# Performance work log

Hardware: AMD Instinct MI355X
Metric: run time of the kernel (lower is better)

Reference implementation:

```python
import jax, jax.numpy as jnp
import numpy as np

DIM = 1024
HIDDEN = 2048
NUM_EXPERTS = 8
TOP_K = 2


def setup_inputs() -> dict:
    key = jax.random.key(0)
    ks = jax.random.split(key, 6)
    scale = 0.02
    x = jax.random.normal(ks[0], (2, 4096, DIM), dtype=jnp.float32)
    # router: Linear(dim, num_experts, bias=False) -> weight [E, d]
    router_w = jax.random.normal(ks[1], (NUM_EXPERTS, DIM), dtype=jnp.float32) * scale
    # per-expert MLP: Linear(d, h) -> w1 [E, h, d], b1 [E, h]; Linear(h, d) -> w2 [E, d, h], b2 [E, d]
    w1 = jax.random.normal(ks[2], (NUM_EXPERTS, HIDDEN, DIM), dtype=jnp.float32) * scale
    b1 = jnp.zeros((NUM_EXPERTS, HIDDEN), dtype=jnp.float32)
    w2 = jax.random.normal(ks[3], (NUM_EXPERTS, DIM, HIDDEN), dtype=jnp.float32) * scale
    b2 = jnp.zeros((NUM_EXPERTS, DIM), dtype=jnp.float32)
    return {"x": x, "router_w": router_w, "w1": w1, "b1": b1, "w2": w2, "b2": b2}


def reference(x, router_w, w1, b1, w2, b2):
    b, s, d = x.shape
    xf = x.reshape(-1, d)                              # [T, d]
    logits = xf @ router_w.T                           # [T, E]
    all_probs = jax.nn.softmax(logits, axis=-1)
    topk_logits, topk_inds = jax.lax.top_k(logits, TOP_K)   # [T, K]
    topk_probs = jax.nn.softmax(topk_logits, axis=-1)
    E = router_w.shape[0]
    onehot = jax.nn.one_hot(topk_inds, E, dtype=xf.dtype)   # [T, K, E]
    # combine weights per (token, expert); zero where expert not selected
    gate = jnp.einsum('tke,tk->te', onehot, topk_probs)     # [T, E]
    # load-balancing auxiliary loss
    f_i = onehot.mean(axis=(0, 1))                          # [E]
    P_i = all_probs.mean(axis=0)                            # [E]
    aux_loss = E * jnp.sum(f_i * P_i)
    # dense per-expert MLP, weighted combine (dropout=0 / eval mode)
    out = jnp.zeros_like(xf)
    for e in range(E):  # fixed small loop over experts
        h = jax.nn.gelu(xf @ w1[e].T + b1[e], approximate=False)  # exact GELU (torch default)
        y = h @ w2[e].T + b2[e]
        out = out + gate[:, e:e + 1] * y
    return out.reshape(b, s, d), aux_loss
```

## Files before the change

### kernel.cpp

```cpp
#include <hip/hip_runtime.h>


#define TOKS 8192
#define DIMD 1024
#define HID  2048
#define NE   8

#define OFF_COUNTS   0
#define OFF_OFFSETS  64
#define OFF_CURSORS  128
#define OFF_TILEOFF  192
#define OFF_TOPKI    256
#define OFF_TOPKG    (OFF_TOPKI + TOKS*2*4)
#define OFF_BLKPS    (OFF_TOPKG + TOKS*2*4)
#define OFF_ATOK     (OFF_BLKPS + 2048*NE*4)
#define OFF_AGATE    (OFF_ATOK + TOKS*2*4)
#define OFF_PINV     (OFF_AGATE + TOKS*2*4)
#define OFF_XG       (1u << 20)
#define XG_ROWS      (TOKS*2 + 256)
#define OFF_W1B      (OFF_XG  + (size_t)XG_ROWS * DIMD * 2)
#define OFF_W2B      (OFF_W1B + (size_t)NE * HID * DIMD * 2)
#define OFF_H        (OFF_W2B + (size_t)NE * DIMD * HID * 2)
#define OFF_Y        (OFF_H   + (size_t)XG_ROWS * HID * 2)

typedef __bf16 bf16x8 __attribute__((ext_vector_type(8)));
typedef float  floatx4 __attribute__((ext_vector_type(4)));

__device__ __forceinline__ float bf2f(unsigned short u) {
    return __uint_as_float(((unsigned)u) << 16);
}
__device__ __forceinline__ unsigned short f2bf(float f) {
    unsigned u = __float_as_uint(f);
    unsigned r = (u + 0x7FFFu + ((u >> 16) & 1u)) >> 16;
    return (unsigned short)r;
}

#define GLOBAL_AS(p) ((const __attribute__((address_space(1))) unsigned int*)(p))
#define LDS_AS(p)    ((__attribute__((address_space(3))) unsigned int*)(p))

__device__ __forceinline__ int xcd_remap(int bid, int nwg) {
    int xcd = bid & 7, pos = bid >> 3;
    int q = nwg >> 3, r = nwg & 7;
    int start = (xcd < r) ? xcd * (q + 1) : r * (q + 1) + (xcd - r) * q;
    return start + pos;
}

__global__ void convert_w_kernel(const float4* __restrict__ w1,
                                 ushort4* __restrict__ w1b, int n1,
                                 const float4* __restrict__ w2,
                                 ushort4* __restrict__ w2b, int n2) {
    int i = blockIdx.x * blockDim.x + threadIdx.x;
    int stride = gridDim.x * blockDim.x;
    int ntot = n1 + n2;
    for (; i < ntot; i += stride) {
        float4 v; ushort4 o;
        if (i < n1) v = w1[i]; else v = w2[i - n1];
        o.x = f2bf(v.x); o.y = f2bf(v.y); o.z = f2bf(v.z); o.w = f2bf(v.w);
        if (i < n1) w1b[i] = o; else w2b[i - n1] = o;
    }
}

__global__ __launch_bounds__(256) void router_kernel(
    const float* __restrict__ x, const float* __restrict__ rw,
    int* __restrict__ topki, float* __restrict__ topkg,
    float* __restrict__ blkps)
{
    int wave = threadIdx.x >> 6;
    int lane = threadIdx.x & 63;
    int t = blockIdx.x * 4 + wave;
    const float* xt = x + (size_t)t * DIMD;

    float acc[NE];
#pragma unroll
    for (int e = 0; e < NE; e++) acc[e] = 0.f;
    for (int i = 0; i < DIMD / 64; i++) {
        float xv = xt[lane + 64 * i];
#pragma unroll
        for (int e = 0; e < NE; e++) acc[e] += xv * rw[e * DIMD + lane + 64 * i];
    }
#pragma unroll
    for (int off = 32; off > 0; off >>= 1) {
#pragma unroll
        for (int e = 0; e < NE; e++) acc[e] += __shfl_down(acc[e], off);
    }

    __shared__ float ps[4][NE];
    if (lane == 0) {
        float m = acc[0];
#pragma unroll
        for (int e = 1; e < NE; e++) m = fmaxf(m, acc[e]);
        float ex[NE], s = 0.f;
#pragma unroll
        for (int e = 0; e < NE; e++) { ex[e] = expf(acc[e] - m); s += ex[e]; }
        float inv = 1.f / s;
#pragma unroll
        for (int e = 0; e < NE; e++) ps[wave][e] = ex[e] * inv;

        int i0 = 0; float l0 = acc[0];
#pragma unroll
        for (int e = 1; e < NE; e++) if (acc[e] > l0) { l0 = acc[e]; i0 = e; }
        int i1 = -1; float l1 = -3.4e38f;
#pragma unroll
        for (int e = 0; e < NE; e++) if (e != i0 && acc[e] > l1) { l1 = acc[e]; i1 = e; }
        float e1 = expf(l1 - l0);
        float g0 = 1.f / (1.f + e1);
        float g1 = e1 * g0;
        topki[t * 2 + 0] = i0; topki[t * 2 + 1] = i1;
        topkg[t * 2 + 0] = g0; topkg[t * 2 + 1] = g1;
    }
    __syncthreads();
    if (threadIdx.x < NE) {
        float s = ps[0][threadIdx.x] + ps[1][threadIdx.x] + ps[2][threadIdx.x] + ps[3][threadIdx.x];
        blkps[blockIdx.x * NE + threadIdx.x] = s;
    }
}

__global__ __launch_bounds__(256) void finalize_kernel(
    const int* __restrict__ topki, const float* __restrict__ blkps,
    int* __restrict__ counts, int* __restrict__ offsets, int* __restrict__ cursors,
    int* __restrict__ tileoff, float* __restrict__ aux_out)
{
    __shared__ float psum[NE];
    __shared__ int cnt[NE];
    int tid = threadIdx.x;
    if (tid < NE) { psum[tid] = 0.f; cnt[tid] = 0; }
    __syncthreads();

    float lp[NE]; int lc[NE];
#pragma unroll
    for (int e = 0; e < NE; e++) { lp[e] = 0.f; lc[e] = 0; }
    const float4* bp4 = (const float4*)blkps;
    for (int i = tid; i < 2048 * NE / 4; i += 256) {
        float4 v = bp4[i];
        int eb = (4 * i) & 7;
        lp[eb + 0] += v.x; lp[eb + 1] += v.y; lp[eb + 2] += v.z; lp[eb + 3] += v.w;
    }
    const int4* ti4 = (const int4*)topki;
    for (int i = tid; i < TOKS * 2 / 4; i += 256) {
        int4 v = ti4[i];
        lc[v.x]++; lc[v.y]++; lc[v.z]++; lc[v.w]++;
    }
#pragma unroll
    for (int e = 0; e < NE; e++) { atomicAdd(&psum[e], lp[e]); atomicAdd(&cnt[e], lc[e]); }
    __syncthreads();

    if (tid == 0) {
        int off = 0, to = 0;
        for (int e = 0; e < NE; e++) {
            counts[e] = cnt[e];
            offsets[e] = off; cursors[e] = off;
            tileoff[e] = to;
            off += cnt[e];
            to += (cnt[e] + 255) >> 8;
        }
        offsets[NE] = off; tileoff[NE] = to;
        float aux = 0.f;
        for (int e = 0; e < NE; e++)
            aux += ((float)cnt[e] / (float)(TOKS * 2)) * (psum[e] / (float)TOKS);
        aux_out[0] = (float)NE * aux;
    }
}

__global__ __launch_bounds__(64) void fill_kernel(
    const int* __restrict__ topki, const float* __restrict__ topkg,
    int* __restrict__ cursors, int* __restrict__ atok, float* __restrict__ agate,
    int* __restrict__ posinv)
{
    int lane = threadIdx.x;
    int t = blockIdx.x * 64 + lane;
    unsigned long long below = (lane == 63) ? 0x7FFFFFFFFFFFFFFFull
                                            : ((1ull << lane) - 1ull);
#pragma unroll
    for (int k = 0; k < 2; k++) {
        int e = topki[t * 2 + k];
        float g = topkg[t * 2 + k];
        for (int ee = 0; ee < NE; ee++) {
            bool pred = (e == ee);
            unsigned long long mask = __ballot(pred ? 1 : 0);
            if (mask) {
                int leader = __ffsll((unsigned long long)mask) - 1;
                int base = 0;
                if (lane == leader) base = atomicAdd(&cursors[ee], (int)__popcll(mask));
                base = __shfl(base, leader);
                if (pred) {
                    int pos = base + (int)__popcll(mask & below);
                    atok[pos] = t;
                    agate[pos] = g;
                    posinv[t * 2 + k] = pos;
                }
            }
        }
    }
}

__global__ __launch_bounds__(256) void gather_x_kernel(
    const float* __restrict__ x, const int* __restrict__ atok,
    ushort* __restrict__ Xg)
{
    int r = blockIdx.x;
    int tid = threadIdx.x;
    int tok = atok[r];
    float4 v = ((const float4*)(x + (size_t)tok * DIMD))[tid];
    ushort4 o;
    o.x = f2bf(v.x); o.y = f2bf(v.y); o.z = f2bf(v.z); o.w = f2bf(v.w);
    ((ushort4*)(Xg + (size_t)r * DIMD))[tid] = o;
}


__global__ __launch_bounds__(512, 2) void phase1_kernel(
    const ushort* __restrict__ Xg, const ushort* __restrict__ w1b,
    const float* __restrict__ b1,
    const int* __restrict__ counts, const int* __restrict__ offsets,
    const int* __restrict__ tileoff, unsigned short* __restrict__ Hbuf)
{
    const int LD = DIMD;
    const int NT = DIMD / 64;
    const int NCOLT = HID / 256;
    int total = tileoff[NE] * NCOLT;
    int idx = xcd_remap((int)blockIdx.x, (int)gridDim.x);
    if (idx >= total) return;
    int ct = idx & (NCOLT - 1);
    int rowt = idx / NCOLT;
    int e = 0;
    while (rowt >= tileoff[e + 1]) e++;
    int row0 = (rowt - tileoff[e]) * 256;
    int cnt = counts[e];
    int base = offsets[e];
    int colbase = ct * 256;

    __shared__ ushort lds[2][64][512];

    int tid = threadIdx.x;
    int lane = tid & 63;
    int wave = tid >> 6;
    int wr = wave >> 2, wc = wave & 3;
    int l15 = lane & 15, quad = lane >> 4;

    const ushort* gApanel = Xg + (size_t)(base + row0) * LD;
    const ushort* gBpanel = w1b + (size_t)e * HID * DIMD + (size_t)colbase * LD;

    const ushort* src[8];
#pragma unroll
    for (int i = 0; i < 8; i++) {
        int chunk = wave * 8 + i;
        int tensor = chunk >> 5;
        int r = chunk & 31;
        int s = r >> 1, h = r & 1;
        const ushort* bse = tensor ? gBpanel : gApanel;
        src[i] = bse + (size_t)(s * 16 + l15) * LD + h * 32 + quad * 8;
    }

#define STAGE(BUF) do { \
    _Pragma("unroll") \
    for (int i = 0; i < 8; i++) { \
        __builtin_amdgcn_global_load_lds(GLOBAL_AS(src[i]), LDS_AS(&lds[BUF][wave*8 + i][0]), 16, 0, 0); \
        src[i] += 64; \
    } \
} while (0)

    floatx4 acc[8][4];
#pragma unroll
    for (int i = 0; i < 8; i++)
#pragma unroll
        for (int j = 0; j < 4; j++) acc[i][j] = (floatx4){0.f, 0.f, 0.f, 0.f};

    auto compute = [&](int bufidx) {
        const bf16x8* C = (const bf16x8*)&lds[bufidx][0][0];
#pragma unroll
        for (int h = 0; h < 2; h++) {
            bf16x8 a[8], b[4];
#pragma unroll
            for (int i = 0; i < 8; i++) a[i] = C[((wr * 8 + i) * 2 + h) * 64 + lane];
#pragma unroll
            for (int j = 0; j < 4; j++) b[j] = C[(32 + (wc * 4 + j) * 2 + h) * 64 + lane];
#pragma unroll
            for (int i = 0; i < 8; i++)
#pragma unroll
                for (int j = 0; j < 4; j++)
                    acc[i][j] = __builtin_amdgcn_mfma_f32_16x16x32_bf16(a[i], b[j], acc[i][j], 0, 0, 0);
        }
    };

    STAGE(0);
    __syncthreads();
    int cur = 0;
    for (int kt = 0; kt < NT - 1; kt++) {
        STAGE(cur ^ 1);
        compute(cur);
        __syncthreads();
        cur ^= 1;
    }
    compute(cur);
#undef STAGE

    float b1v[4];
#pragma unroll
    for (int j = 0; j < 4; j++)
        b1v[j] = b1[e * HID + colbase + 64 * wc + 16 * j + l15];
#pragma unroll
    for (int i = 0; i < 8; i++) {
#pragma unroll
        for (int rr = 0; rr < 4; rr++) {
            int pr = row0 + 128 * wr + 16 * i + quad * 4 + rr;
            if (pr < cnt) {
                size_t hrow = (size_t)(base + pr) * HID;
#pragma unroll
                for (int j = 0; j < 4; j++) {
                    int col = colbase + 64 * wc + 16 * j + l15;
                    float v = acc[i][j][rr] + b1v[j];
                    v = 0.5f * v * (1.f + erff(v * 0.70710678118654752f));
                    Hbuf[hrow + col] = f2bf(v);
                }
            }
        }
    }
}

__global__ __launch_bounds__(512, 2) void phase2_kernel(
    const ushort* __restrict__ Hbuf, const ushort* __restrict__ w2b,
    const int* __restrict__ counts, const int* __restrict__ offsets,
    const int* __restrict__ tileoff, ushort* __restrict__ Y)
{
    const int LD = HID;
    const int NT = HID / 64;
    const int NCOLT = DIMD / 256;
    int total = tileoff[NE] * NCOLT;
    int idx = xcd_remap((int)blockIdx.x, (int)gridDim.x);
    if (idx >= total) return;
    int ct = idx & (NCOLT - 1);
    int rowt = idx / NCOLT;
    int e = 0;
    while (rowt >= tileoff[e + 1]) e++;
    int row0 = (rowt - tileoff[e]) * 256;
    int cnt = counts[e];
    int base = offsets[e];
    int colbase = ct * 256;

    __shared__ ushort lds[2][64][512];

    int tid = threadIdx.x;
    int lane = tid & 63;
    int wave = tid >> 6;
    int wr = wave >> 2, wc = wave & 3;
    int l15 = lane & 15, quad = lane >> 4;

    const ushort* gApanel = Hbuf + (size_t)(base + row0) * LD;
    const ushort* gBpanel = w2b + (size_t)e * DIMD * HID + (size_t)colbase * LD;

    const ushort* src[8];
#pragma unroll
    for (int i = 0; i < 8; i++) {
        int chunk = wave * 8 + i;
        int tensor = chunk >> 5;
        int r = chunk & 31;
        int s = r >> 1, h = r & 1;
        const ushort* bse = tensor ? gBpanel : gApanel;
        src[i] = bse + (size_t)(s * 16 + l15) * LD + h * 32 + quad * 8;
    }

#define STAGE(BUF) do { \
    _Pragma("unroll") \
    for (int i = 0; i < 8; i++) { \
        __builtin_amdgcn_global_load_lds(GLOBAL_AS(src[i]), LDS_AS(&lds[BUF][wave*8 + i][0]), 16, 0, 0); \
        src[i] += 64; \
    } \
} while (0)

    floatx4 acc[8][4];
#pragma unroll
    for (int i = 0; i < 8; i++)
#pragma unroll
        for (int j = 0; j < 4; j++) acc[i][j] = (floatx4){0.f, 0.f, 0.f, 0.f};

    auto compute = [&](int bufidx) {
        const bf16x8* C = (const bf16x8*)&lds[bufidx][0][0];
#pragma unroll
        for (int h = 0; h < 2; h++) {
            bf16x8 a[8], b[4];
#pragma unroll
            for (int i = 0; i < 8; i++) a[i] = C[((wr * 8 + i) * 2 + h) * 64 + lane];
#pragma unroll
            for (int j = 0; j < 4; j++) b[j] = C[(32 + (wc * 4 + j) * 2 + h) * 64 + lane];
#pragma unroll
            for (int i = 0; i < 8; i++)
#pragma unroll
                for (int j = 0; j < 4; j++)
                    acc[i][j] = __builtin_amdgcn_mfma_f32_16x16x32_bf16(a[i], b[j], acc[i][j], 0, 0, 0);
        }
    };

    STAGE(0);
    __syncthreads();
    int cur = 0;
    for (int kt = 0; kt < NT - 1; kt++) {
        STAGE(cur ^ 1);
        compute(cur);
        __syncthreads();
        cur ^= 1;
    }
    compute(cur);
#undef STAGE

#pragma unroll
    for (int i = 0; i < 8; i++) {
#pragma unroll
        for (int rr = 0; rr < 4; rr++) {
            int pr = row0 + 128 * wr + 16 * i + quad * 4 + rr;
            if (pr < cnt) {
                size_t yrow = (size_t)(base + pr) * DIMD;
#pragma unroll
                for (int j = 0; j < 4; j++) {
                    int col = colbase + 64 * wc + 16 * j + l15;
                    Y[yrow + col] = f2bf(acc[i][j][rr]);
                }
            }
        }
    }
}

__global__ __launch_bounds__(256) void combine_kernel(
    const ushort* __restrict__ Y, const float* __restrict__ b2,
    const int* __restrict__ topki, const float* __restrict__ topkg,
    const int* __restrict__ posinv, float* __restrict__ out)
{
    int wave = threadIdx.x >> 6;
    int lane = threadIdx.x & 63;
    int t = blockIdx.x * 4 + wave;
    int e0 = topki[t * 2 + 0], e1 = topki[t * 2 + 1];
    float g0 = topkg[t * 2 + 0], g1 = topkg[t * 2 + 1];
    int p0 = posinv[t * 2 + 0], p1 = posinv[t * 2 + 1];

    const ushort4* y0 = (const ushort4*)(Y + (size_t)p0 * DIMD);
    const ushort4* y1 = (const ushort4*)(Y + (size_t)p1 * DIMD);
    const float4* b20 = (const float4*)(b2 + (size_t)e0 * DIMD);
    const float4* b21 = (const float4*)(b2 + (size_t)e1 * DIMD);
    float4* o4 = (float4*)(out + (size_t)t * DIMD);

#pragma unroll
    for (int c = 0; c < DIMD / 4 / 64; c++) {
        int i = lane + 64 * c;
        ushort4 a = y0[i], b = y1[i];
        float4 ba = b20[i], bb = b21[i];
        float4 r;
        r.x = g0 * (bf2f(a.x) + ba.x) + g1 * (bf2f(b.x) + bb.x);
        r.y = g0 * (bf2f(a.y) + ba.y) + g1 * (bf2f(b.y) + bb.y);
        r.z = g0 * (bf2f(a.z) + ba.z) + g1 * (bf2f(b.z) + bb.z);
        r.w = g0 * (bf2f(a.w) + ba.w) + g1 * (bf2f(b.w) + bb.w);
        o4[i] = r;
    }
}

extern "C" void kernel_launch(void* const* d_in, const int* in_sizes, int n_in,
                              void* d_out, int out_size, void* d_ws, size_t ws_size,
                              hipStream_t stream) {
    const float* x  = (const float*)d_in[0];
    const float* rw = (const float*)d_in[1];
    const float* w1 = (const float*)d_in[2];
    const float* b1 = (const float*)d_in[3];
    const float* w2 = (const float*)d_in[4];
    const float* b2 = (const float*)d_in[5];
    float* out = (float*)d_out;

    char* ws = (char*)d_ws;
    int*   counts  = (int*)(ws + OFF_COUNTS);
    int*   offsets = (int*)(ws + OFF_OFFSETS);
    int*   cursors = (int*)(ws + OFF_CURSORS);
    int*   tileoff = (int*)(ws + OFF_TILEOFF);
    int*   topki   = (int*)(ws + OFF_TOPKI);
    float* topkg   = (float*)(ws + OFF_TOPKG);
    float* blkps   = (float*)(ws + OFF_BLKPS);
    int*   atok    = (int*)(ws + OFF_ATOK);
    float* agate   = (float*)(ws + OFF_AGATE);
    int*   posinv  = (int*)(ws + OFF_PINV);
    ushort* Xg     = (ushort*)(ws + OFF_XG);
    ushort* w1b    = (ushort*)(ws + OFF_W1B);
    ushort* w2b    = (ushort*)(ws + OFF_W2B);
    ushort* Hbuf   = (ushort*)(ws + OFF_H);
    ushort* Y      = (ushort*)(ws + OFF_Y);

    convert_w_kernel<<<8192, 256, 0, stream>>>(
        (const float4*)w1, (ushort4*)w1b, NE * HID * DIMD / 4,
        (const float4*)w2, (ushort4*)w2b, NE * DIMD * HID / 4);

    router_kernel<<<TOKS / 4, 256, 0, stream>>>(x, rw, topki, topkg, blkps);
    finalize_kernel<<<1, 256, 0, stream>>>(topki, blkps, counts, offsets, cursors,
                                           tileoff, out + (size_t)TOKS * DIMD);
    fill_kernel<<<TOKS / 64, 64, 0, stream>>>(topki, topkg, cursors, atok, agate,
                                              posinv);
    gather_x_kernel<<<TOKS * 2, 256, 0, stream>>>(x, atok, Xg);

    phase1_kernel<<<71 * (HID / 256), 512, 0, stream>>>(
        Xg, w1b, b1, counts, offsets, tileoff, Hbuf);
    phase2_kernel<<<71 * (DIMD / 256), 512, 0, stream>>>(
        Hbuf, w2b, counts, offsets, tileoff, Y);
    combine_kernel<<<TOKS / 4, 256, 0, stream>>>(Y, b2, topki, topkg, posinv, out);
}
```

Baseline: 629.3 us.

## Replace double-buffered GEMM mainloop with eight-phase interleaved load/MFMA schedule

Both expert GEMM kernels now share a templated mainloop that splits each K-tile into four quadrant phases. Each phase issues part of the next tile's global-to-LDS loads and runs the MFMA work for one sub-quadrant, with explicit s_barrier, waitcnt, sched_barrier and setprio control. The goal is finer overlap of memory traffic with matrix-core work and less idle time at the single barrier per tile. In exchange there are many more barriers and hand-tuned vmcnt counts, which are fragile and could cause stalls or races if the wait counts are wrong.

```diff
diff --git a/kernel.cpp b/kernel.cpp
--- a/kernel.cpp
+++ b/kernel.cpp
@@ -206,6 +206,87 @@
     ((ushort4*)(Xg + (size_t)r * DIMD))[tid] = o;
 }
 
+template<int LD, int NT>
+__device__ __forceinline__ void gemm8ph(
+    const ushort* __restrict__ gApanel, const ushort* __restrict__ gBpanel,
+    ushort (&lds)[2][64][512], floatx4 (&acc)[8][4],
+    int lane, int wave, int wr, int wc, int l15, int quad)
+{
+    const bf16x8* C0 = (const bf16x8*)&lds[0][0][0];
+    const bf16x8* C1 = (const bf16x8*)&lds[1][0][0];
+
+    auto stage_half = [&](int bsel, int hf, int u) {
+        const ushort* panel = (hf & 2) ? gBpanel : gApanel;
+        int rbase = (hf & 1) * 128 + wave * 16 + l15;
+        const ushort* s0 = panel + (size_t)rbase * LD + u * 64 + quad * 8;
+        __builtin_amdgcn_global_load_lds(GLOBAL_AS(s0),
+            LDS_AS(&lds[bsel][hf * 16 + wave * 2 + 0][0]), 16, 0, 0);
+        __builtin_amdgcn_global_load_lds(GLOBAL_AS(s0 + 32),
+            LDS_AS(&lds[bsel][hf * 16 + wave * 2 + 1][0]), 16, 0, 0);
+    };
+
+#pragma unroll
+    for (int i = 0; i < 8; i++)
+#pragma unroll
+        for (int j = 0; j < 4; j++) acc[i][j] = (floatx4){0.f, 0.f, 0.f, 0.f};
+
+    bf16x8 af[4][2], bf[2][2];
+
+#define PH(CB, MH, NH, RA, RB, DOSTAGE, SB, SHF, SU, DOWAIT, DEEP)            \
+    {                                                                          \
+        if (RA) {                                                              \
+            _Pragma("unroll") for (int mi = 0; mi < 4; mi++) {                 \
+                af[mi][0] = CB[((wr * 8 + (MH)*4 + mi) * 2 + 0) * 64 + lane];  \
+                af[mi][1] = CB[((wr * 8 + (MH)*4 + mi) * 2 + 1) * 64 + lane];  \
+            }                                                                  \
+        }                                                                      \
+        if (RB) {                                                              \
+            _Pragma("unroll") for (int nj = 0; nj < 2; nj++) {                 \
+                bf[nj][0] = CB[(32 + (wc * 4 + (NH)*2 + nj) * 2 + 0) * 64 + lane]; \
+                bf[nj][1] = CB[(32 + (wc * 4 + (NH)*2 + nj) * 2 + 1) * 64 + lane]; \
+            }                                                                  \
+        }                                                                      \
+        if (DOSTAGE) stage_half(SB, SHF, SU);                                  \
+        __builtin_amdgcn_s_barrier();                                          \
+        asm volatile("s_waitcnt lgkmcnt(0)" ::: "memory");                     \
+        __builtin_amdgcn_sched_barrier(0);                                     \
+        __builtin_amdgcn_s_setprio(1);                                         \
+        _Pragma("unroll") for (int mi = 0; mi < 4; mi++)                       \
+            _Pragma("unroll") for (int nj = 0; nj < 2; nj++)                   \
+                _Pragma("unroll") for (int kk = 0; kk < 2; kk++)               \
+                    acc[(MH)*4 + mi][(NH)*2 + nj] =                            \
+                        __builtin_amdgcn_mfma_f32_16x16x32_bf16(               \
+                            af[mi][kk], bf[nj][kk],                            \
+                            acc[(MH)*4 + mi][(NH)*2 + nj], 0, 0, 0);           \
+        __builtin_amdgcn_s_setprio(0);                                         \
+        if (DOWAIT) {                                                          \
+            if (DEEP) asm volatile("s_waitcnt vmcnt(0)" ::: "memory");         \
+            else      asm volatile("s_waitcnt vmcnt(4)" ::: "memory");         \
+        }                                                                      \
+        __builtin_amdgcn_s_barrier();                                          \
+    }
+
+    stage_half(0, 0, 0);
+    stage_half(0, 2, 0);
+    stage_half(0, 3, 0);
+    stage_half(0, 1, 0);
+    stage_half(1, 0, 1);
+    stage_half(1, 3, 1);
+    asm volatile("s_waitcnt vmcnt(4)" ::: "memory");
+    __builtin_amdgcn_s_barrier();
+
+    for (int u = 0; u < NT; u += 2) {
+        PH(C0, 0, 0, 1, 1, (u + 1 < NT), 1, 1, u + 1, 0, 0);
+        PH(C0, 0, 1, 0, 1, (u + 1 < NT), 1, 2, u + 1, 0, 0);
+        PH(C0, 1, 1, 1, 0, (u + 2 < NT), 0, 0, u + 2, 0, 0);
+        PH(C0, 1, 0, 0, 1, (u + 2 < NT), 0, 3, u + 2, 1, (u + 2 >= NT));
+        PH(C1, 0, 0, 1, 1, (u + 2 < NT), 0, 1, u + 2, 0, 0);
+        PH(C1, 0, 1, 0, 1, (u + 2 < NT), 0, 2, u + 2, 0, 0);
+        PH(C1, 1, 1, 1, 0, (u + 3 < NT), 1, 0, u + 3, 0, 0);
+        PH(C1, 1, 0, 0, 1, (u + 3 < NT), 1, 3, u + 3, 1, (u + 3 >= NT));
+    }
+#undef PH
+}
 
 __global__ __launch_bounds__(512, 2) void phase1_kernel(
     const ushort* __restrict__ Xg, const ushort* __restrict__ w1b,
@@ -213,8 +294,6 @@
     const int* __restrict__ counts, const int* __restrict__ offsets,
     const int* __restrict__ tileoff, unsigned short* __restrict__ Hbuf)
 {
-    const int LD = DIMD;
-    const int NT = DIMD / 64;
     const int NCOLT = HID / 256;
     int total = tileoff[NE] * NCOLT;
     int idx = xcd_remap((int)blockIdx.x, (int)gridDim.x);
@@ -236,62 +315,11 @@
     int wr = wave >> 2, wc = wave & 3;
     int l15 = lane & 15, quad = lane >> 4;
 
-    const ushort* gApanel = Xg + (size_t)(base + row0) * LD;
-    const ushort* gBpanel = w1b + (size_t)e * HID * DIMD + (size_t)colbase * LD;
-
-    const ushort* src[8];
-#pragma unroll
-    for (int i = 0; i < 8; i++) {
-        int chunk = wave * 8 + i;
-        int tensor = chunk >> 5;
-        int r = chunk & 31;
-        int s = r >> 1, h = r & 1;
-        const ushort* bse = tensor ? gBpanel : gApanel;
-        src[i] = bse + (size_t)(s * 16 + l15) * LD + h * 32 + quad * 8;
-    }
-
-#define STAGE(BUF) do { \
-    _Pragma("unroll") \
-    for (int i = 0; i < 8; i++) { \
-        __builtin_amdgcn_global_load_lds(GLOBAL_AS(src[i]), LDS_AS(&lds[BUF][wave*8 + i][0]), 16, 0, 0); \
-        src[i] += 64; \
-    } \
-} while (0)
+    const ushort* gApanel = Xg + (size_t)(base + row0) * DIMD;
+    const ushort* gBpanel = w1b + (size_t)e * HID * DIMD + (size_t)colbase * DIMD;
 
     floatx4 acc[8][4];
-#pragma unroll
-    for (int i = 0; i < 8; i++)
-#pragma unroll
-        for (int j = 0; j < 4; j++) acc[i][j] = (floatx4){0.f, 0.f, 0.f, 0.f};
-
-    auto compute = [&](int bufidx) {
-        const bf16x8* C = (const bf16x8*)&lds[bufidx][0][0];
-#pragma unroll
-        for (int h = 0; h < 2; h++) {
-            bf16x8 a[8], b[4];
-#pragma unroll
-            for (int i = 0; i < 8; i++) a[i] = C[((wr * 8 + i) * 2 + h) * 64 + lane];
-#pragma unroll
-            for (int j = 0; j < 4; j++) b[j] = C[(32 + (wc * 4 + j) * 2 + h) * 64 + lane];
-#pragma unroll
-            for (int i = 0; i < 8; i++)
-#pragma unroll
-                for (int j = 0; j < 4; j++)
-                    acc[i][j] = __builtin_amdgcn_mfma_f32_16x16x32_bf16(a[i], b[j], acc[i][j], 0, 0, 0);
-        }
-    };
-
-    STAGE(0);
-    __syncthreads();
-    int cur = 0;
-    for (int kt = 0; kt < NT - 1; kt++) {
-        STAGE(cur ^ 1);
-        compute(cur);
-        __syncthreads();
-        cur ^= 1;
-    }
-    compute(cur);
-#undef STAGE
+    gemm8ph<DIMD, DIMD / 64>(gApanel, gBpanel, lds, acc, lane, wave, wr, wc, l15, quad);
 
     float b1v[4];
 #pragma unroll
@@ -321,8 +349,6 @@
     const int* __restrict__ counts, const int* __restrict__ offsets,
     const int* __restrict__ tileoff, ushort* __restrict__ Y)
 {
-    const int LD = HID;
-    const int NT = HID / 64;
     const int NCOLT = DIMD / 256;
     int total = tileoff[NE] * NCOLT;
     int idx = xcd_remap((int)blockIdx.x, (int)gridDim.x);
@@ -344,62 +370,11 @@
     int wr = wave >> 2, wc = wave & 3;
     int l15 = lane & 15, quad = lane >> 4;
 
-    const ushort* gApanel = Hbuf + (size_t)(base + row0) * LD;
-    const ushort* gBpanel = w2b + (size_t)e * DIMD * HID + (size_t)colbase * LD;
-
-    const ushort* src[8];
-#pragma unroll
-    for (int i = 0; i < 8; i++) {
-        int chunk = wave * 8 + i;
-        int tensor = chunk >> 5;
-        int r = chunk & 31;
-        int s = r >> 1, h = r & 1;
-        const ushort* bse = tensor ? gBpanel : gApanel;
-        src[i] = bse + (size_t)(s * 16 + l15) * LD + h * 32 + quad * 8;
-    }
-
-#define STAGE(BUF) do { \
-    _Pragma("unroll") \
-    for (int i = 0; i < 8; i++) { \
-        __builtin_amdgcn_global_load_lds(GLOBAL_AS(src[i]), LDS_AS(&lds[BUF][wave*8 + i][0]), 16, 0, 0); \
-        src[i] += 64; \
-    } \
-} while (0)
+    const ushort* gApanel = Hbuf + (size_t)(base + row0) * HID;
+    const ushort* gBpanel = w2b + (size_t)e * DIMD * HID + (size_t)colbase * HID;
 
     floatx4 acc[8][4];
-#pragma unroll
-    for (int i = 0; i < 8; i++)
-#pragma unroll
-        for (int j = 0; j < 4; j++) acc[i][j] = (floatx4){0.f, 0.f, 0.f, 0.f};
-
-    auto compute = [&](int bufidx) {
-        const bf16x8* C = (const bf16x8*)&lds[bufidx][0][0];
-#pragma unroll
-        for (int h = 0; h < 2; h++) {
-            bf16x8 a[8], b[4];
-#pragma unroll
-            for (int i = 0; i < 8; i++) a[i] = C[((wr * 8 + i) * 2 + h) * 64 + lane];
-#pragma unroll
-            for (int j = 0; j < 4; j++) b[j] = C[(32 + (wc * 4 + j) * 2 + h) * 64 + lane];
-#pragma unroll
-            for (int i = 0; i < 8; i++)
-#pragma unroll
-                for (int j = 0; j < 4; j++)
-                    acc[i][j] = __builtin_amdgcn_mfma_f32_16x16x32_bf16(a[i], b[j], acc[i][j], 0, 0, 0);
-        }
-    };
-
-    STAGE(0);
-    __syncthreads();
-    int cur = 0;
-    for (int kt = 0; kt < NT - 1; kt++) {
-        STAGE(cur ^ 1);
-        compute(cur);
-        __syncthreads();
-        cur ^= 1;
-    }
-    compute(cur);
-#undef STAGE
+    gemm8ph<HID, HID / 64>(gApanel, gBpanel, lds, acc, lane, wave, wr, wc, l15, quad);
 
 #pragma unroll
     for (int i = 0; i < 8; i++) {
```

After: 591.3 us. 1.06x faster.
